# Performance work log

Hardware: AMD Instinct MI355X
Metric: run time of the kernel (lower is better)

## Reference

```python
import jax, jax.numpy as jnp
import numpy as np

B, T_V, T_A = 128, 64, 128
E_V, E_A = 1024, 512
H, EMB, C = 1024, 512, 512  # C = input_size - embedding_size
IN = EMB + C               # RNN input size = 1024
VOCAB = 20000


def setup_inputs() -> dict:
    key = jax.random.key(0)
    ks = jax.random.split(key, 26)
    s = 0.02
    inp = {
        "input": jax.random.normal(ks[0], (B, 1, EMB), jnp.float32),
        "enc_visual": jax.random.normal(ks[1], (B, T_V, E_V), jnp.float32),
        "enc_audio": jax.random.normal(ks[2], (B, T_A, E_A), jnp.float32),
        "hidden_state": jax.random.normal(ks[3], (1, B, H), jnp.float32),
        "cell_state": jax.random.normal(ks[4], (1, B, H), jnp.float32),
        # visual attention (Bahdanau): W1:[C,H], W2:[C,E_V], W3:[1,C]
        "W_va1": s * jax.random.normal(ks[5], (C, H), jnp.float32),
        "W_va2": s * jax.random.normal(ks[6], (C, E_V), jnp.float32),
        "W_va3": s * jax.random.normal(ks[7], (1, C), jnp.float32),
        "W_venc": s * jax.random.normal(ks[8], (C, E_V), jnp.float32),
        # audio attention
        "W_aa1": s * jax.random.normal(ks[9], (C, H), jnp.float32),
        "W_aa2": s * jax.random.normal(ks[10], (C, E_A), jnp.float32),
        "W_aa3": s * jax.random.normal(ks[11], (1, C), jnp.float32),
        "W_aenc": s * jax.random.normal(ks[12], (C, E_A), jnp.float32),
        # cross-modal context attention (over 2 context vectors)
        "W_ca1": s * jax.random.normal(ks[13], (C, H), jnp.float32),
        "W_ca2": s * jax.random.normal(ks[14], (C, C), jnp.float32),
        "W_ca3": s * jax.random.normal(ks[15], (1, C), jnp.float32),
        # LSTM-style custom RNN cell params
        "W_ih": s * jax.random.normal(ks[16], (4 * H, IN), jnp.float32),
        "W_hh": s * jax.random.normal(ks[17], (4 * H, H), jnp.float32),
        "b_ih": jnp.zeros((4 * H,), jnp.float32),
        "b_hh": jnp.zeros((4 * H,), jnp.float32),
        # output projection
        "W_out": s * jax.random.normal(ks[18], (VOCAB, H), jnp.float32),
        "b_out": jnp.zeros((VOCAB,), jnp.float32),
    }
    return inp


def _attend(h, enc, W1, W2, W3):
    # h: [B,H]; enc: [B,T,E]. Vectorized Bahdanau attention (original loops over T).
    v1 = h @ W1.T                               # [B,C]
    v2 = jnp.einsum('bte,ce->btc', enc, W2)     # [B,T,C]
    scores = jnp.tanh(v1[:, None, :] + v2) @ W3.T  # [B,T,1]
    attn = jax.nn.softmax(scores[..., 0], axis=1)  # [B,T]
    return jnp.einsum('bt,bte->be', attn, enc)     # [B,E]


def reference(input, enc_visual, enc_audio, hidden_state, cell_state,
              W_va1, W_va2, W_va3, W_venc,
              W_aa1, W_aa2, W_aa3, W_aenc,
              W_ca1, W_ca2, W_ca3,
              W_ih, W_hh, b_ih, b_hh, W_out, b_out):
    h0 = hidden_state[0]   # [B,H]
    c0 = cell_state[0]     # [B,H]

    vc = _attend(h0, enc_visual, W_va1, W_va2, W_va3) @ W_venc.T  # [B,C]
    ac = _attend(h0, enc_audio, W_aa1, W_aa2, W_aa3) @ W_aenc.T   # [B,C]
    all_ctx = jnp.stack([vc, ac], axis=1)                         # [B,2,C]
    final_ctx = _attend(h0, all_ctx, W_ca1, W_ca2, W_ca3)         # [B,C]

    x = jnp.concatenate([input[:, 0, :], jnp.tanh(final_ctx)], axis=-1)  # [B,IN]
    gates = x @ W_ih.T + b_ih + h0 @ W_hh.T + b_hh                 # [B,4H]
    i, f, g, o = jnp.split(gates, 4, axis=-1)
    c_new = jax.nn.sigmoid(f) * c0 + jax.nn.sigmoid(i) * jnp.tanh(g)
    h_new = jax.nn.sigmoid(o) * jnp.tanh(c_new)

    logits = h_new @ W_out.T + b_out                               # [B,V]
    return (logits[:, None, :], h_new[None], c_new[None])
```

## Files before the change

### kernel.cpp

```cpp
#include <hip/hip_runtime.h>
#include <hip/hip_bf16.h>
#include <cstddef>

typedef __attribute__((ext_vector_type(8))) short short8;
typedef __attribute__((ext_vector_type(4))) float f32x4;

static __device__ __forceinline__ f32x4 ldg(const float* p) {
    return *(const f32x4*)p;
}

static __device__ __forceinline__ short8 pack8(f32x4 f0, f32x4 f1) {
    union { __hip_bfloat162 h[4]; short8 s; } u;
    u.h[0] = __float22bfloat162_rn(make_float2(f0.x, f0.y));
    u.h[1] = __float22bfloat162_rn(make_float2(f0.z, f0.w));
    u.h[2] = __float22bfloat162_rn(make_float2(f1.x, f1.y));
    u.h[3] = __float22bfloat162_rn(make_float2(f1.z, f1.w));
    return u.s;
}

static __device__ __forceinline__ void gload16(const short* g, short* l) {
    __builtin_amdgcn_global_load_lds(
        (const __attribute__((address_space(1))) void*)g,
        (__attribute__((address_space(3))) void*)l, 16, 0, 0);
}

static __device__ __forceinline__ void lds_barrier() {
    asm volatile("s_waitcnt lgkmcnt(0)" ::: "memory");
    __builtin_amdgcn_s_barrier();
    asm volatile("" ::: "memory");
}

static __device__ __forceinline__ void sk_body(
    const float* __restrict__ A, int lda,
    const float* __restrict__ W,
    const float* __restrict__ bias, int addbias,
    float* __restrict__ C, int ldc, int N,
    int kbeg, int kend, int n0, int m0)
{
    __shared__ short As[2][128 * 32];
    __shared__ short Ws[2][64 * 32];
    const int tid  = threadIdx.x;
    const int lane = tid & 63;
    const int wave = tid >> 6;
    const int wm = wave * 32;

    f32x4 acc[2][4];
    #pragma unroll
    for (int i = 0; i < 2; ++i)
        #pragma unroll
        for (int j = 0; j < 4; ++j)
            acc[i][j] = (f32x4){0.f, 0.f, 0.f, 0.f};

    const int arow = tid >> 1;
    const int ah   = tid & 1;
    const int afs  = (arow >> 1) & 3;
    const float* gA = A + (size_t)(m0 + arow) * lda + kbeg + ah * 16;
    const int aoff0 = arow * 32 + (((ah * 2)     ^ afs) * 8);
    const int aoff1 = arow * 32 + (((ah * 2 + 1) ^ afs) * 8);

    const int wrow  = tid >> 2;
    const int wslot = tid & 3;
    const int wvalid = (n0 + wrow) < N;
    const float* gW = W + (size_t)(n0 + wrow) * lda + kbeg + wslot * 8;
    const int woff = wrow * 32 + ((wslot ^ ((wrow >> 1) & 3)) * 8);

    const int frow = lane & 15;
    const int hi   = lane >> 4;
    const int fsl  = (hi ^ ((frow >> 1) & 3)) * 8;
    const int ra   = (wm + frow) * 32 + fsl;
    const int rb   = frow * 32 + fsl;

    const int nsteps = (kend - kbeg) >> 5;

    f32x4 a0_[4], a1_[4], w0_[2], w1_[2];
    #pragma unroll
    for (int q = 0; q < 4; ++q) a0_[q] = ldg(gA + q * 4);
    #pragma unroll
    for (int q = 0; q < 4; ++q) a1_[q] = ldg(gA + 32 + q * 4);
    if (wvalid) {
        w0_[0] = ldg(gW);      w0_[1] = ldg(gW + 4);
        w1_[0] = ldg(gW + 32); w1_[1] = ldg(gW + 36);
    } else {
        w0_[0] = w0_[1] = w1_[0] = w1_[1] = (f32x4){0.f, 0.f, 0.f, 0.f};
    }

    for (int s = 0; s < nsteps; s += 2) {
        {
            short* as = As[0]; short* ws = Ws[0];
            *(short8*)(as + aoff0) = pack8(a0_[0], a0_[1]);
            *(short8*)(as + aoff1) = pack8(a0_[2], a0_[3]);
            *(short8*)(ws + woff)  = pack8(w0_[0], w0_[1]);
            if (s + 2 < nsteps) {
                const float* nA = gA + (s + 2) * 32;
                #pragma unroll
                for (int q = 0; q < 4; ++q) a0_[q] = ldg(nA + q * 4);
                if (wvalid) {
                    const float* nW = gW + (s + 2) * 32;
                    w0_[0] = ldg(nW); w0_[1] = ldg(nW + 4);
                }
            }
            lds_barrier();
            short8 af[2], bf[4];
            #pragma unroll
            for (int i = 0; i < 2; ++i) af[i] = *(const short8*)(as + ra + i * 512);
            #pragma unroll
            for (int j = 0; j < 4; ++j) bf[j] = *(const short8*)(ws + rb + j * 512);
            #pragma unroll
            for (int i = 0; i < 2; ++i)
                #pragma unroll
                for (int j = 0; j < 4; ++j)
                    acc[i][j] = __builtin_amdgcn_mfma_f32_16x16x32_bf16(af[i], bf[j], acc[i][j], 0, 0, 0);
        }
        {
            short* as = As[1]; short* ws = Ws[1];
            *(short8*)(as + aoff0) = pack8(a1_[0], a1_[1]);
            *(short8*)(as + aoff1) = pack8(a1_[2], a1_[3]);
            *(short8*)(ws + woff)  = pack8(w1_[0], w1_[1]);
            if (s + 3 < nsteps) {
                const float* nA = gA + (s + 3) * 32;
                #pragma unroll
                for (int q = 0; q < 4; ++q) a1_[q] = ldg(nA + q * 4);
                if (wvalid) {
                    const float* nW = gW + (s + 3) * 32;
                    w1_[0] = ldg(nW); w1_[1] = ldg(nW + 4);
                }
            }
            lds_barrier();
            short8 af[2], bf[4];
            #pragma unroll
            for (int i = 0; i < 2; ++i) af[i] = *(const short8*)(as + ra + i * 512);
            #pragma unroll
            for (int j = 0; j < 4; ++j) bf[j] = *(const short8*)(ws + rb + j * 512);
            #pragma unroll
            for (int i = 0; i < 2; ++i)
                #pragma unroll
                for (int j = 0; j < 4; ++j)
                    acc[i][j] = __builtin_amdgcn_mfma_f32_16x16x32_bf16(af[i], bf[j], acc[i][j], 0, 0, 0);
        }
    }

    const int cl = lane & 15;
    const int rq = hi * 4;
    #pragma unroll
    for (int j = 0; j < 4; ++j) {
        int gc = n0 + j * 16 + cl;
        if (gc >= N) continue;
        float b = addbias ? bias[gc] : 0.f;
        #pragma unroll
        for (int i = 0; i < 2; ++i) {
            int gr = m0 + wm + i * 16 + rq;
            #pragma unroll
            for (int r = 0; r < 4; ++r)
                atomicAdd(C + (size_t)(gr + r) * ldc + gc, acc[i][j][r] + b);
        }
    }
}

__global__ __launch_bounds__(256) void gemm_sk(
    const float* __restrict__ A, const float* __restrict__ W,
    const float* __restrict__ bias, float* __restrict__ C,
    int N, int K, int kchunk, int ldc)
{
    int kbeg = blockIdx.y * kchunk;
    sk_body(A, K, W, bias, bias != nullptr && blockIdx.y == 0,
            C, ldc, N, kbeg, kbeg + kchunk, blockIdx.x * 64, blockIdx.z * 128);
}

__global__ __launch_bounds__(256) void hproj3_mfma(
    const float* __restrict__ h0,
    const float* __restrict__ Wa, const float* __restrict__ Wb, const float* __restrict__ Wc,
    float* __restrict__ hbase)
{
    int n0g = blockIdx.x * 64;
    int wsel = n0g >> 9;
    const float* W = (wsel == 0) ? Wa : (wsel == 1) ? Wb : Wc;
    float* C = hbase + (size_t)wsel * 128 * 512;
    int kbeg = blockIdx.y * 128;
    sk_body(h0, 1024, W, nullptr, 0, C, 512, 512, kbeg, kbeg + 128, n0g & 511, 0);
}

__global__ __launch_bounds__(256) void ctxproj_mfma(
    const float* __restrict__ attv, const float* __restrict__ Wv,
    const float* __restrict__ atta, const float* __restrict__ Wa,
    float* __restrict__ ctx)
{
    const float* A; const float* W; float* C; int lda, kb, ke;
    if (blockIdx.z == 0) { A = attv; W = Wv; C = ctx;       lda = 1024; kb = blockIdx.y * 128; ke = kb + 128; }
    else                 { A = atta; W = Wa; C = ctx + 512; lda = 512;  kb = blockIdx.y * 64;  ke = kb + 64;  }
    sk_body(A, lda, W, nullptr, 0, C, 1024, 512, kb, ke, blockIdx.x * 64, 0);
}

__global__ __launch_bounds__(256) void gates_mfma(
    const float* __restrict__ xb, const float* __restrict__ W_ih,
    const float* __restrict__ h0, const float* __restrict__ W_hh,
    float* __restrict__ gates)
{
    int pair = blockIdx.y >> 2;
    const float* A = pair ? h0 : xb;
    const float* W = pair ? W_hh : W_ih;
    int kb = (blockIdx.y & 3) * 256;
    sk_body(A, 1024, W, nullptr, 0, gates, 4096, 4096, kb, kb + 256, blockIdx.x * 64, 0);
}

__global__ __launch_bounds__(256) void cvt_bf16(
    const float* __restrict__ encv, const float* __restrict__ enca,
    const float* __restrict__ wv2,  const float* __restrict__ wa2,
    short* __restrict__ oev, short* __restrict__ oea,
    short* __restrict__ owv, short* __restrict__ owa)
{
    int bid = blockIdx.x;
    const float* src; short* dst; int lb;
    if (bid < 4096)      { src = encv; dst = oev; lb = bid; }
    else if (bid < 8192) { src = enca; dst = oea; lb = bid - 4096; }
    else if (bid < 8448) { src = wv2;  dst = owv; lb = bid - 8192; }
    else                 { src = wa2;  dst = owa; lb = bid - 8448; }
    size_t off = ((size_t)lb * 256 + threadIdx.x) * 8;
    f32x4 f0 = *(const f32x4*)(src + off);
    f32x4 f1 = *(const f32x4*)(src + off + 4);
    *(short8*)(dst + off) = pack8(f0, f1);
}

__global__ __launch_bounds__(256) void scores_fused(
    const short* __restrict__ Av, const short* __restrict__ Wv,
    const float* __restrict__ hv1,  const float* __restrict__ W_va3,
    float* __restrict__ scv,
    const short* __restrict__ Aa, const short* __restrict__ Wa,
    const float* __restrict__ ha1,  const float* __restrict__ W_aa3,
    float* __restrict__ sca)
{
    __shared__ short As[2][4096];
    __shared__ short Ws[2][4096];

    const short *A, *W; const float *v1, *W3;
    float* sc;
    int K, tshift, n0, m0;
    int idx = blockIdx.x;
    if (idx < 256) {
        n0 = (idx >> 6) * 128;  m0 = (idx & 63) * 128;
        A = Av; W = Wv; v1 = hv1; W3 = W_va3; sc = scv;
        K = 1024; tshift = 6;
    } else {
        idx -= 256;
        n0 = (idx >> 7) * 128;  m0 = (idx & 127) * 128;
        A = Aa; W = Wa; v1 = ha1; W3 = W_aa3; sc = sca;
        K = 512; tshift = 7;
    }

    const int tid  = threadIdx.x;
    const int lane = tid & 63;
    const int wave = tid >> 6;
    const int wr = wave >> 1;
    const int wc = wave & 1;

    f32x4 acc[4][4];
    #pragma unroll
    for (int i = 0; i < 4; ++i)
        #pragma unroll
        for (int j = 0; j < 4; ++j)
            acc[i][j] = (f32x4){0.f, 0.f, 0.f, 0.f};

    const int srow = lane >> 2;
    const int slsw = (lane & 3) ^ ((lane >> 3) & 3);
    const short* gA0 = A + (size_t)(m0 + wave * 16 + srow) * K + slsw * 8;
    const short* gA1 = gA0 + (size_t)64 * K;
    const short* gW0 = W + (size_t)(n0 + wave * 16 + srow) * K + slsw * 8;
    const short* gW1 = gW0 + (size_t)64 * K;
    const int ldsw = wave * 512;

    const int frow = lane & 15;
    const int hi   = lane >> 4;
    const int fsl  = (hi ^ ((frow >> 1) & 3)) * 8;
    const int raBase = (wr * 64 + frow) * 32 + fsl;
    const int rbBase = (wc * 64 + frow) * 32 + fsl;

    const int nsteps = K >> 5;

    gload16(gA0, As[0] + ldsw);
    gload16(gA1, As[0] + 2048 + ldsw);
    gload16(gW0, Ws[0] + ldsw);
    gload16(gW1, Ws[0] + 2048 + ldsw);

    int cur = 0;
    for (int s = 0; s < nsteps; ++s) {
        int nk = (s + 1 < nsteps ? s + 1 : s) * 32;
        gload16(gA0 + nk, As[cur ^ 1] + ldsw);
        gload16(gA1 + nk, As[cur ^ 1] + 2048 + ldsw);
        gload16(gW0 + nk, Ws[cur ^ 1] + ldsw);
        gload16(gW1 + nk, Ws[cur ^ 1] + 2048 + ldsw);
        asm volatile("s_waitcnt vmcnt(4)" ::: "memory");
        __builtin_amdgcn_s_barrier();
        __builtin_amdgcn_sched_barrier(0);

        const short* as = As[cur];
        const short* ws = Ws[cur];
        short8 af[4], bf[4];
        #pragma unroll
        for (int i = 0; i < 4; ++i) af[i] = *(const short8*)(as + raBase + i * 512);
        #pragma unroll
        for (int j = 0; j < 4; ++j) bf[j] = *(const short8*)(ws + rbBase + j * 512);
        #pragma unroll
        for (int i = 0; i < 4; ++i)
            #pragma unroll
            for (int j = 0; j < 4; ++j)
                acc[i][j] = __builtin_amdgcn_mfma_f32_16x16x32_bf16(af[i], bf[j], acc[i][j], 0, 0, 0);
        __builtin_amdgcn_sched_barrier(0);
        __builtin_amdgcn_s_barrier();
        cur ^= 1;
    }

    const int cl = lane & 15;
    const int rq = hi * 4;
    #pragma unroll
    for (int i = 0; i < 4; ++i) {
        #pragma unroll
        for (int r = 0; r < 4; ++r) {
            int gr = m0 + wr * 64 + i * 16 + rq + r;
            const float* v1row = v1 + (size_t)(gr >> tshift) * 512;
            float p = 0.f;
            #pragma unroll
            for (int j = 0; j < 4; ++j) {
                int gc = n0 + wc * 64 + j * 16 + cl;
                p += tanhf(v1row[gc] + acc[i][j][r]) * W3[gc];
            }
            p += __shfl_xor(p, 1, 64);
            p += __shfl_xor(p, 2, 64);
            p += __shfl_xor(p, 4, 64);
            p += __shfl_xor(p, 8, 64);
            if (cl == 0) atomicAdd(sc + gr, p);
        }
    }
}

__global__ __launch_bounds__(256) void attend_out2(
    const float* __restrict__ scv, const float* __restrict__ encv, float* __restrict__ attv,
    const float* __restrict__ sca, const float* __restrict__ enca, float* __restrict__ atta)
{
    const float* sc; const float* enc; float* out;
    int T, E, ec;
    if (blockIdx.y < 4) { sc = scv; enc = encv; out = attv; T = 64;  E = 1024; ec = blockIdx.y; }
    else                { sc = sca; enc = enca; out = atta; T = 128; E = 512;  ec = blockIdx.y - 4; }

    __shared__ float ew[128];
    const int b = blockIdx.x, tid = threadIdx.x;
    __shared__ float raw[128];
    if (tid < T) raw[tid] = sc[(size_t)b * T + tid];
    __syncthreads();
    float m = -1e30f;
    for (int t = 0; t < T; ++t) m = fmaxf(m, raw[t]);
    if (tid < T) ew[tid] = __expf(raw[tid] - m);
    __syncthreads();
    float sum = 0.f;
    for (int t = 0; t < T; ++t) sum += ew[t];
    const float inv = 1.f / sum;

    const int e = ec * 256 + tid;
    const float* encb = enc + (size_t)b * T * E + e;
    float acc = 0.f;
    for (int t = 0; t < T; ++t)
        acc += ew[t] * encb[(size_t)t * E];
    out[(size_t)b * E + e] = acc * inv;
}

__global__ __launch_bounds__(256) void cross_kernel(
    const float* __restrict__ hc1, const float* __restrict__ v2c,
    const float* __restrict__ W3, const float* __restrict__ ctx,
    const float* __restrict__ inp, float* __restrict__ x)
{
    const int C = 512;
    __shared__ float red[256];
    __shared__ float aw[2];
    const int b = blockIdx.x, tid = threadIdx.x;

    float p0 = 0.f, p1 = 0.f;
    for (int c = tid; c < C; c += 256) {
        float h = hc1[(size_t)b * C + c], w = W3[c];
        p0 += tanhf(h + v2c[(size_t)(b * 2 + 0) * C + c]) * w;
        p1 += tanhf(h + v2c[(size_t)(b * 2 + 1) * C + c]) * w;
    }
    red[tid] = p0; __syncthreads();
    for (int s = 128; s; s >>= 1) { if (tid < s) red[tid] += red[tid + s]; __syncthreads(); }
    float s0 = red[0];
    __syncthreads();
    red[tid] = p1; __syncthreads();
    for (int s = 128; s; s >>= 1) { if (tid < s) red[tid] += red[tid + s]; __syncthreads(); }
    if (tid == 0) {
        float s1 = red[0];
        float m = fmaxf(s0, s1);
        float e0 = __expf(s0 - m), e1 = __expf(s1 - m);
        float inv = 1.f / (e0 + e1);
        aw[0] = e0 * inv; aw[1] = e1 * inv;
    }
    __syncthreads();
    float a0 = aw[0], a1 = aw[1];
    for (int c = tid; c < C; c += 256) {
        float fc = a0 * ctx[(size_t)(b * 2 + 0) * C + c]
                 + a1 * ctx[(size_t)(b * 2 + 1) * C + c];
        x[(size_t)b * 1024 + 512 + c] = tanhf(fc);
        x[(size_t)b * 1024 + c] = inp[(size_t)b * 512 + c];
    }
}

__global__ __launch_bounds__(256) void lstm_kernel(
    const float* __restrict__ gates, const float* __restrict__ c0,
    const float* __restrict__ b_ih, const float* __restrict__ b_hh,
    float* __restrict__ hout, float* __restrict__ cout)
{
    const int idx = blockIdx.x * 256 + threadIdx.x;
    const int b = idx >> 10, h = idx & 1023;
    const float* g = gates + (size_t)b * 4096;
    float gi = g[h]        + b_ih[h]        + b_hh[h];
    float gf = g[1024 + h] + b_ih[1024 + h] + b_hh[1024 + h];
    float gg = g[2048 + h] + b_ih[2048 + h] + b_hh[2048 + h];
    float go = g[3072 + h] + b_ih[3072 + h] + b_hh[3072 + h];
    float si = 1.f / (1.f + __expf(-gi));
    float sf = 1.f / (1.f + __expf(-gf));
    float so = 1.f / (1.f + __expf(-go));
    float cn = sf * c0[idx] + si * tanhf(gg);
    float hn = so * tanhf(cn);
    cout[idx] = cn;
    hout[idx] = hn;
}

extern "C" void kernel_launch(void* const* d_in, const int* in_sizes, int n_in,
                              void* d_out, int out_size, void* d_ws, size_t ws_size,
                              hipStream_t stream)
{
    const float* inp    = (const float*)d_in[0];
    const float* encv   = (const float*)d_in[1];
    const float* enca   = (const float*)d_in[2];
    const float* h0     = (const float*)d_in[3];
    const float* c0     = (const float*)d_in[4];
    const float* W_va1  = (const float*)d_in[5];
    const float* W_va2  = (const float*)d_in[6];
    const float* W_va3  = (const float*)d_in[7];
    const float* W_venc = (const float*)d_in[8];
    const float* W_aa1  = (const float*)d_in[9];
    const float* W_aa2  = (const float*)d_in[10];
    const float* W_aa3  = (const float*)d_in[11];
    const float* W_aenc = (const float*)d_in[12];
    const float* W_ca1  = (const float*)d_in[13];
    const float* W_ca2  = (const float*)d_in[14];
    const float* W_ca3  = (const float*)d_in[15];
    const float* W_ih   = (const float*)d_in[16];
    const float* W_hh   = (const float*)d_in[17];
    const float* b_ih   = (const float*)d_in[18];
    const float* b_hh   = (const float*)d_in[19];
    const float* W_out  = (const float*)d_in[20];
    const float* b_out  = (const float*)d_in[21];
    float* out = (float*)d_out;

    float* ws = (float*)d_ws;
    float* hv1  = ws;  ws += 128 * 512;
    float* ha1  = ws;  ws += 128 * 512;
    float* hc1  = ws;  ws += 128 * 512;
    float* scv  = ws;  ws += 128 * 64;
    float* sca  = ws;  ws += 128 * 128;
    float* ctx  = ws;  ws += 128 * 2 * 512;
    float* v2c  = ws;  ws += 128 * 2 * 512;
    float* gates= ws;  ws += (size_t)128 * 4096;
    size_t zero_floats = (size_t)(ws - (float*)d_ws);
    float* xb   = ws;  ws += 128 * 1024;
    float* attv = ws;  ws += 128 * 1024;
    float* atta = ws;  ws += 128 * 512;
    short* encv_bf = (short*)ws;  ws += 8388608 / 2;
    short* enca_bf = (short*)ws;  ws += 8388608 / 2;
    short* wv2_bf  = (short*)ws;  ws += 524288 / 2;
    short* wa2_bf  = (short*)ws;  ws += 262144 / 2;

    dim3 blk(256);

    hipMemsetAsync(d_ws, 0, zero_floats * sizeof(float), stream);
    hipMemsetAsync(out, 0, (size_t)128 * 20000 * sizeof(float), stream);

    cvt_bf16<<<dim3(8576), blk, 0, stream>>>(encv, enca, W_va2, W_aa2,
                                             encv_bf, enca_bf, wv2_bf, wa2_bf);
    hproj3_mfma<<<dim3(24, 8), blk, 0, stream>>>(h0, W_va1, W_aa1, W_ca1, hv1);
    scores_fused<<<dim3(768), blk, 0, stream>>>(encv_bf, wv2_bf, hv1, W_va3, scv,
                                                enca_bf, wa2_bf, ha1, W_aa3, sca);
    attend_out2<<<dim3(128, 6), blk, 0, stream>>>(scv, encv, attv, sca, enca, atta);
    ctxproj_mfma<<<dim3(8, 8, 2), blk, 0, stream>>>(attv, W_venc, atta, W_aenc, ctx);
    gemm_sk<<<dim3(8, 4, 2), blk, 0, stream>>>(ctx, W_ca2, nullptr, v2c, 512, 512, 128, 512);
    cross_kernel<<<128, blk, 0, stream>>>(hc1, v2c, W_ca3, ctx, inp, xb);
    gates_mfma<<<dim3(64, 8), blk, 0, stream>>>(xb, W_ih, h0, W_hh, gates);
    float* hout = out + 2560000;
    float* cout = out + 2560000 + 131072;
    lstm_kernel<<<512, blk, 0, stream>>>(gates, c0, b_ih, b_hh, hout, cout);
    gemm_sk<<<dim3(313, 2, 1), blk, 0, stream>>>(hout, W_out, b_out, out, 20000, 1024, 512, 20000);
}
```

Baseline: 374.6 us.

## Fuse hproj into bf16 convert, triple-buffer scores, read bf16 enc in attend

Merges the h-projection GEMM into the bf16 conversion kernel so one launch does both. Deepens the scores GEMM LDS pipeline from double to triple buffering with a looser vmcnt wait. The attention-output kernel now reads the bf16 copies of the encoder tensors, halving its traffic, at the cost of bf16 rounding in the weighted sum. The sk_body weight pointer arithmetic is also split into separate terms.

```diff
diff --git a/kernel.cpp b/kernel.cpp
--- a/kernel.cpp
+++ b/kernel.cpp
@@ -24,6 +24,13 @@
         (__attribute__((address_space(3))) void*)l, 16, 0, 0);
 }
 
+static __device__ __forceinline__ float bflo(unsigned int u) {
+    union { unsigned int i; float f; } c; c.i = u << 16; return c.f;
+}
+static __device__ __forceinline__ float bfhi(unsigned int u) {
+    union { unsigned int i; float f; } c; c.i = u & 0xffff0000u; return c.f;
+}
+
 static __device__ __forceinline__ void lds_barrier() {
     asm volatile("s_waitcnt lgkmcnt(0)" ::: "memory");
     __builtin_amdgcn_s_barrier();
@@ -61,7 +68,7 @@
     const int wrow  = tid >> 2;
     const int wslot = tid & 3;
     const int wvalid = (n0 + wrow) < N;
-    const float* gW = W + (size_t)(n0 + wrow) * lda + kbeg + wslot * 8;
+    const float* gW = W + (size_t)n0 * lda + (size_t)wrow * lda + kbeg + wslot * 8;
     const int woff = wrow * 32 + ((wslot ^ ((wrow >> 1) & 3)) * 8);
 
     const int frow = lane & 15;
@@ -166,19 +173,6 @@
             C, ldc, N, kbeg, kbeg + kchunk, blockIdx.x * 64, blockIdx.z * 128);
 }
 
-__global__ __launch_bounds__(256) void hproj3_mfma(
-    const float* __restrict__ h0,
-    const float* __restrict__ Wa, const float* __restrict__ Wb, const float* __restrict__ Wc,
-    float* __restrict__ hbase)
-{
-    int n0g = blockIdx.x * 64;
-    int wsel = n0g >> 9;
-    const float* W = (wsel == 0) ? Wa : (wsel == 1) ? Wb : Wc;
-    float* C = hbase + (size_t)wsel * 128 * 512;
-    int kbeg = blockIdx.y * 128;
-    sk_body(h0, 1024, W, nullptr, 0, C, 512, 512, kbeg, kbeg + 128, n0g & 511, 0);
-}
-
 __global__ __launch_bounds__(256) void ctxproj_mfma(
     const float* __restrict__ attv, const float* __restrict__ Wv,
     const float* __restrict__ atta, const float* __restrict__ Wa,
@@ -202,22 +196,35 @@
     sk_body(A, 1024, W, nullptr, 0, gates, 4096, 4096, kb, kb + 256, blockIdx.x * 64, 0);
 }
 
-__global__ __launch_bounds__(256) void cvt_bf16(
+__global__ __launch_bounds__(256) void cvt_hproj(
     const float* __restrict__ encv, const float* __restrict__ enca,
     const float* __restrict__ wv2,  const float* __restrict__ wa2,
     short* __restrict__ oev, short* __restrict__ oea,
-    short* __restrict__ owv, short* __restrict__ owa)
+    short* __restrict__ owv, short* __restrict__ owa,
+    const float* __restrict__ h0,
+    const float* __restrict__ Wva1, const float* __restrict__ Waa1,
+    const float* __restrict__ Wca1, float* __restrict__ hbase)
 {
     int bid = blockIdx.x;
-    const float* src; short* dst; int lb;
-    if (bid < 4096)      { src = encv; dst = oev; lb = bid; }
-    else if (bid < 8192) { src = enca; dst = oea; lb = bid - 4096; }
-    else if (bid < 8448) { src = wv2;  dst = owv; lb = bid - 8192; }
-    else                 { src = wa2;  dst = owa; lb = bid - 8448; }
-    size_t off = ((size_t)lb * 256 + threadIdx.x) * 8;
-    f32x4 f0 = *(const f32x4*)(src + off);
-    f32x4 f1 = *(const f32x4*)(src + off + 4);
-    *(short8*)(dst + off) = pack8(f0, f1);
+    if (bid < 8576) {
+        const float* src; short* dst; int lb;
+        if (bid < 4096)      { src = encv; dst = oev; lb = bid; }
+        else if (bid < 8192) { src = enca; dst = oea; lb = bid - 4096; }
+        else if (bid < 8448) { src = wv2;  dst = owv; lb = bid - 8192; }
+        else                 { src = wa2;  dst = owa; lb = bid - 8448; }
+        size_t off = ((size_t)lb * 256 + threadIdx.x) * 8;
+        f32x4 f0 = *(const f32x4*)(src + off);
+        f32x4 f1 = *(const f32x4*)(src + off + 4);
+        *(short8*)(dst + off) = pack8(f0, f1);
+        return;
+    }
+    int lb = bid - 8576;
+    int n0g = (lb % 24) * 64;
+    int kid = lb / 24;
+    int wsel = n0g >> 9;
+    const float* W = (wsel == 0) ? Wva1 : (wsel == 1) ? Waa1 : Wca1;
+    float* C = hbase + (size_t)wsel * 128 * 512;
+    sk_body(h0, 1024, W, nullptr, 0, C, 512, 512, kid * 128, kid * 128 + 128, n0g & 511, 0);
 }
 
 __global__ __launch_bounds__(256) void scores_fused(
@@ -228,8 +235,8 @@
     const float* __restrict__ ha1,  const float* __restrict__ W_aa3,
     float* __restrict__ sca)
 {
-    __shared__ short As[2][4096];
-    __shared__ short Ws[2][4096];
+    __shared__ short As[3][4096];
+    __shared__ short Ws[3][4096];
 
     const short *A, *W; const float *v1, *W3;
     float* sc;
@@ -275,24 +282,28 @@
 
     const int nsteps = K >> 5;
 
-    gload16(gA0, As[0] + ldsw);
-    gload16(gA1, As[0] + 2048 + ldsw);
-    gload16(gW0, Ws[0] + ldsw);
-    gload16(gW1, Ws[0] + 2048 + ldsw);
-
-    int cur = 0;
+    short* A0 = &As[0][0];
+    short* W0 = &Ws[0][0];
+    auto stage = [&](int buf, int koff) {
+        gload16(gA0 + koff, A0 + buf * 4096 + ldsw);
+        gload16(gA1 + koff, A0 + buf * 4096 + 2048 + ldsw);
+        gload16(gW0 + koff, W0 + buf * 4096 + ldsw);
+        gload16(gW1 + koff, W0 + buf * 4096 + 2048 + ldsw);
+    };
+
+    stage(0, 0);
+    stage(1, 32);
+
+    int b0 = 0, b1 = 1, b2 = 2;
     for (int s = 0; s < nsteps; ++s) {
-        int nk = (s + 1 < nsteps ? s + 1 : s) * 32;
-        gload16(gA0 + nk, As[cur ^ 1] + ldsw);
-        gload16(gA1 + nk, As[cur ^ 1] + 2048 + ldsw);
-        gload16(gW0 + nk, Ws[cur ^ 1] + ldsw);
-        gload16(gW1 + nk, Ws[cur ^ 1] + 2048 + ldsw);
-        asm volatile("s_waitcnt vmcnt(4)" ::: "memory");
+        int kk = s + 2; if (kk > nsteps - 1) kk = nsteps - 1;
+        stage(b2, kk * 32);
+        asm volatile("s_waitcnt vmcnt(8)" ::: "memory");
         __builtin_amdgcn_s_barrier();
         __builtin_amdgcn_sched_barrier(0);
 
-        const short* as = As[cur];
-        const short* ws = Ws[cur];
+        const short* as = A0 + b0 * 4096;
+        const short* ws = W0 + b0 * 4096;
         short8 af[4], bf[4];
         #pragma unroll
         for (int i = 0; i < 4; ++i) af[i] = *(const short8*)(as + raBase + i * 512);
@@ -305,7 +316,7 @@
                 acc[i][j] = __builtin_amdgcn_mfma_f32_16x16x32_bf16(af[i], bf[j], acc[i][j], 0, 0, 0);
         __builtin_amdgcn_sched_barrier(0);
         __builtin_amdgcn_s_barrier();
-        cur ^= 1;
+        int t = b0; b0 = b1; b1 = b2; b2 = t;
     }
 
     const int cl = lane & 15;
@@ -332,17 +343,19 @@
 }
 
 __global__ __launch_bounds__(256) void attend_out2(
-    const float* __restrict__ scv, const float* __restrict__ encv, float* __restrict__ attv,
-    const float* __restrict__ sca, const float* __restrict__ enca, float* __restrict__ atta)
-{
-    const float* sc; const float* enc; float* out;
-    int T, E, ec;
-    if (blockIdx.y < 4) { sc = scv; enc = encv; out = attv; T = 64;  E = 1024; ec = blockIdx.y; }
-    else                { sc = sca; enc = enca; out = atta; T = 128; E = 512;  ec = blockIdx.y - 4; }
+    const float* __restrict__ scv, const short* __restrict__ encv_bf, float* __restrict__ attv,
+    const float* __restrict__ sca, const short* __restrict__ enca_bf, float* __restrict__ atta)
+{
+    const float* sc; const unsigned int* enc2; float* out;
+    int T, E2, ec;
+    if (blockIdx.y < 2) { sc = scv; enc2 = (const unsigned int*)encv_bf; out = attv;
+                          T = 64;  E2 = 512; ec = blockIdx.y; }
+    else                { sc = sca; enc2 = (const unsigned int*)enca_bf; out = atta;
+                          T = 128; E2 = 256; ec = 0; }
 
     __shared__ float ew[128];
+    __shared__ float raw[128];
     const int b = blockIdx.x, tid = threadIdx.x;
-    __shared__ float raw[128];
     if (tid < T) raw[tid] = sc[(size_t)b * T + tid];
     __syncthreads();
     float m = -1e30f;
@@ -353,12 +366,17 @@
     for (int t = 0; t < T; ++t) sum += ew[t];
     const float inv = 1.f / sum;
 
-    const int e = ec * 256 + tid;
-    const float* encb = enc + (size_t)b * T * E + e;
-    float acc = 0.f;
-    for (int t = 0; t < T; ++t)
-        acc += ew[t] * encb[(size_t)t * E];
-    out[(size_t)b * E + e] = acc * inv;
+    const int ep = ec * 256 + tid;
+    const unsigned int* encb = enc2 + (size_t)b * T * E2 + ep;
+    float a0 = 0.f, a1 = 0.f;
+    for (int t = 0; t < T; ++t) {
+        unsigned int u = encb[(size_t)t * E2];
+        float w = ew[t];
+        a0 += w * bflo(u);
+        a1 += w * bfhi(u);
+    }
+    out[(size_t)b * E2 * 2 + ep * 2]     = a0 * inv;
+    out[(size_t)b * E2 * 2 + ep * 2 + 1] = a1 * inv;
 }
 
 __global__ __launch_bounds__(256) void cross_kernel(
@@ -472,12 +490,12 @@
     hipMemsetAsync(d_ws, 0, zero_floats * sizeof(float), stream);
     hipMemsetAsync(out, 0, (size_t)128 * 20000 * sizeof(float), stream);
 
-    cvt_bf16<<<dim3(8576), blk, 0, stream>>>(encv, enca, W_va2, W_aa2,
-                                             encv_bf, enca_bf, wv2_bf, wa2_bf);
-    hproj3_mfma<<<dim3(24, 8), blk, 0, stream>>>(h0, W_va1, W_aa1, W_ca1, hv1);
+    cvt_hproj<<<dim3(8768), blk, 0, stream>>>(encv, enca, W_va2, W_aa2,
+                                              encv_bf, enca_bf, wv2_bf, wa2_bf,
+                                              h0, W_va1, W_aa1, W_ca1, hv1);
     scores_fused<<<dim3(768), blk, 0, stream>>>(encv_bf, wv2_bf, hv1, W_va3, scv,
                                                 enca_bf, wa2_bf, ha1, W_aa3, sca);
-    attend_out2<<<dim3(128, 6), blk, 0, stream>>>(scv, encv, attv, sca, enca, atta);
+    attend_out2<<<dim3(128, 3), blk, 0, stream>>>(scv, encv_bf, attv, sca, enca_bf, atta);
     ctxproj_mfma<<<dim3(8, 8, 2), blk, 0, stream>>>(attv, W_venc, atta, W_aenc, ctx);
     gemm_sk<<<dim3(8, 4, 2), blk, 0, stream>>>(ctx, W_ca2, nullptr, v2c, 512, 512, 128, 512);
     cross_kernel<<<128, blk, 0, stream>>>(hc1, v2c, W_ca3, ctx, inp, xb);
```

Result: no change. 377.4 us (+0.7%).
